# Optimization experiments

Measured on AMD Instinct MI355X. Metric: run time of the kernel, lower is better.

The kernel has to match this reference:

```python
import jax, jax.numpy as jnp
import numpy as np

DIM_CAP = 16   # capsule dim
NCLS = 17      # annotation_nr
BS = 16
T = 120        # chunk_size * fps
P = 22         # players per frame graph
G = BS * T     # number of graphs = 1920
N = G * P      # nodes = 42240
C_IN = 14
CHS = [16, 32, 64, 152]  # 8m,16m,32m,76m with m=2
BN_EPS = 1e-3


def _build_graph():
    # fully-connected directed edges within each 22-node graph (no self loops)
    ii, jj = np.meshgrid(np.arange(P), np.arange(P), indexing='ij')
    mask = ii != jj
    li, lj = ii[mask], jj[mask]               # (462,)
    base = (np.arange(G) * P)[:, None]
    src = (base + li[None, :]).reshape(-1)
    dst = (base + lj[None, :]).reshape(-1)
    edge_index = np.stack([src, dst]).astype(np.int64)   # (2, E)
    batch = np.repeat(np.arange(G), P).astype(np.int64)  # (N,)
    return jnp.asarray(edge_index), jnp.asarray(batch)


def setup_inputs() -> dict:
    key = jax.random.key(0)
    ks = jax.random.split(key, 16)
    edge_index, batch = _build_graph()
    E = edge_index.shape[1]
    x = jax.random.normal(ks[0], (N, C_IN), dtype=jnp.float32)
    edge_attr = jax.random.uniform(ks[1], (E, 5), dtype=jnp.float32)
    dims = [C_IN] + CHS
    params = {}
    for i in range(4):
        s = 1.0 / np.sqrt(dims[i])
        params[f'W{i+1}'] = jax.random.normal(ks[2 + i], (dims[i], dims[i + 1]), dtype=jnp.float32) * s
        params[f'b{i+1}'] = jnp.zeros((dims[i + 1],), dtype=jnp.float32)
    c_out = DIM_CAP * NCLS  # 272
    params['conv_w'] = jax.random.normal(ks[6], (c_out, CHS[-1], 3), dtype=jnp.float32) * (1.0 / np.sqrt(CHS[-1] * 3))
    params['conv_b'] = jnp.zeros((c_out,), dtype=jnp.float32)
    params['bn_gamma'] = jnp.ones((T,), dtype=jnp.float32)
    params['bn_beta'] = jnp.zeros((T,), dtype=jnp.float32)
    return dict(x=x, edge_index=edge_index, batch=batch, edge_attr=edge_attr, **params)


def _gcn_layer(x, src, dst, w_edge, W, b):
    # PyG GCNConv: x' = D^-1/2 (A + I) D^-1/2 (x W) + b, edge weights w, self-loop weight 1
    n = x.shape[0]
    h = x @ W
    loop = jnp.arange(n)
    src_f = jnp.concatenate([src, loop])
    dst_f = jnp.concatenate([dst, loop])
    w_f = jnp.concatenate([w_edge, jnp.ones((n,), h.dtype)])
    deg = jax.ops.segment_sum(w_f, dst_f, num_segments=n)
    dinv = jnp.where(deg > 0, jax.lax.rsqrt(deg), 0.0)
    norm = dinv[src_f] * w_f * dinv[dst_f]
    out = jax.ops.segment_sum(norm[:, None] * h[src_f], dst_f, num_segments=n)
    return out + b


def reference(x, edge_index, batch, edge_attr, W1, b1, W2, b2, W3, b3, W4, b4,
              conv_w, conv_b, bn_gamma, bn_beta):
    src, dst = edge_index[0], edge_index[1]
    ew = edge_attr[:, 4]
    h = jax.nn.relu(_gcn_layer(x, src, dst, ew, W1, b1))
    h = jax.nn.relu(_gcn_layer(h, src, dst, ew, W2, b2))
    h = jax.nn.relu(_gcn_layer(h, src, dst, ew, W3, b3))
    h = jax.nn.relu(_gcn_layer(h, src, dst, ew, W4, b4))
    # global mean pool per graph -> (G, 152)
    ones = jnp.ones((h.shape[0],), h.dtype)
    cnt = jax.ops.segment_sum(ones, batch, num_segments=G)
    pooled = jax.ops.segment_sum(h, batch, num_segments=G) / jnp.clip(cnt, 1.0)[:, None]
    # (BS, T, 152) -> (BS, 152, T); conv kernel (3,1) with pad (1,1) on T
    feat = pooled.reshape(BS, T, CHS[-1]).transpose(0, 2, 1)
    conv = jax.lax.conv_general_dilated(
        feat, conv_w, window_strides=(1,), padding=[(1, 1)],
        dimension_numbers=('NCH', 'OIH', 'NCH'))
    conv = conv + conv_b[None, :, None]            # (BS, 272, T)
    caps = conv.transpose(0, 2, 1).reshape(BS, T, DIM_CAP, NCLS)
    # BatchNorm2d(num_features=T) in eval mode: running mean 0, var 1
    scale = (bn_gamma / jnp.sqrt(1.0 + BN_EPS))[None, :, None, None]
    shift = bn_beta[None, :, None, None]
    s = jax.nn.sigmoid(caps * scale + shift)
    out = jnp.sqrt(jnp.sum(jnp.square(s - 0.5), axis=2) * 4.0 / DIM_CAP)
    return out  # (BS, T, NCLS)
```

## Files before the change

### kernel.cpp

```cpp
#include <hip/hip_runtime.h>
#include <hip/hip_bf16.h>

#define P22 22
#define PP 24
#define GROUPS 1920
#define CH4 152

template<int DIN, int DOUT, int PR1, int CR1, int PR2, int CR2>
__device__ __forceinline__ void gcn_layer(const float* __restrict__ W,
                                          const float* __restrict__ B,
                                          float* buf, float* T,
                                          const float* M, int tid)
{
    constexpr int NCT1 = DOUT / CR1;
    constexpr int NPT1 = PP / PR1;
    static_assert(NCT1 * NPT1 <= 256, "phase1 tiles must fit one round");
    if (tid < NCT1 * NPT1) {
        const int pt = tid / NCT1, ct = tid - pt * NCT1;
        const int p0 = pt * PR1, c0 = ct * CR1;
        float acc[PR1][CR1];
        #pragma unroll
        for (int a = 0; a < PR1; ++a)
            #pragma unroll
            for (int b = 0; b < CR1; ++b) acc[a][b] = 0.f;
        #pragma unroll 2
        for (int k = 0; k < DIN; ++k) {
            float xv[PR1], wv[CR1];
            #pragma unroll
            for (int a = 0; a < PR1; ++a) xv[a] = buf[k * PP + p0 + a];
            #pragma unroll
            for (int b = 0; b < CR1; ++b) wv[b] = W[k * DOUT + c0 + b];
            #pragma unroll
            for (int a = 0; a < PR1; ++a)
                #pragma unroll
                for (int b = 0; b < CR1; ++b)
                    acc[a][b] = fmaf(xv[a], wv[b], acc[a][b]);
        }
        #pragma unroll
        for (int a = 0; a < PR1; ++a)
            #pragma unroll
            for (int b = 0; b < CR1; ++b)
                T[(p0 + a) * DOUT + c0 + b] = acc[a][b];
    }
    __syncthreads();

    constexpr int NPT2 = PP / PR2;
    constexpr int NCT2 = DOUT / CR2;
    static_assert(NPT2 * NCT2 <= 256, "phase2 tiles must fit one round");
    if (tid < NPT2 * NCT2) {
        const int ct = tid / NPT2, pt = tid - ct * NPT2;
        const int p0 = pt * PR2, c0 = ct * CR2;
        float acc[CR2][PR2];
        #pragma unroll
        for (int b = 0; b < CR2; ++b) {
            const float bias = B[c0 + b];
            #pragma unroll
            for (int a = 0; a < PR2; ++a) acc[b][a] = bias;
        }
        #pragma unroll 2
        for (int q = 0; q < P22; ++q) {
            float av[PR2], tv[CR2];
            #pragma unroll
            for (int a = 0; a < PR2; ++a) av[a] = M[q * PP + p0 + a];
            #pragma unroll
            for (int b = 0; b < CR2; ++b) tv[b] = T[q * DOUT + c0 + b];
            #pragma unroll
            for (int b = 0; b < CR2; ++b)
                #pragma unroll
                for (int a = 0; a < PR2; ++a)
                    acc[b][a] = fmaf(av[a], tv[b], acc[b][a]);
        }
        #pragma unroll
        for (int b = 0; b < CR2; ++b)
            #pragma unroll
            for (int a = 0; a < PR2; ++a)
                buf[(c0 + b) * PP + p0 + a] = fmaxf(acc[b][a], 0.f);
    }
    __syncthreads();
}

__global__ __launch_bounds__(256) void gcn_kernel(
    const float* __restrict__ x, const float* __restrict__ ea,
    const float* __restrict__ W1, const float* __restrict__ b1,
    const float* __restrict__ W2, const float* __restrict__ b2,
    const float* __restrict__ W3, const float* __restrict__ b3,
    const float* __restrict__ W4, const float* __restrict__ b4,
    float* __restrict__ pooled)
{
    __shared__ __align__(16) float M[PP * PP];
    __shared__ __align__(16) float dinv[PP];
    __shared__ __align__(16) float buf[CH4 * PP];
    __shared__ __align__(16) float T[PP * CH4];

    const int g = blockIdx.x, tid = threadIdx.x;

    for (int idx = tid; idx < PP * PP; idx += 256) {
        int i = idx / PP, j = idx - i * PP;
        float v = 0.f;
        if (i < P22 && j < P22) {
            if (i == j) v = 1.0f;
            else {
                int e = i * 21 + j - (j > i);
                v = ea[((size_t)g * 462 + e) * 5 + 4];
            }
        }
        M[idx] = v;
    }
    for (int idx = tid; idx < 14 * PP; idx += 256) {
        int k = idx / PP, p = idx - k * PP;
        buf[idx] = (p < P22) ? x[((size_t)g * P22 + p) * 14 + k] : 0.f;
    }
    __syncthreads();

    if (tid < PP) {
        float s = 0.f;
        #pragma unroll
        for (int i = 0; i < P22; ++i) s += M[i * PP + tid];
        dinv[tid] = (s > 0.f) ? rsqrtf(s) : 0.f;
    }
    __syncthreads();
    for (int e = tid; e < PP * PP; e += 256) {
        int i = e / PP, j = e - i * PP;
        M[e] *= dinv[i] * dinv[j];
    }
    __syncthreads();

    gcn_layer<14, 16,  1, 2, 2, 1>(W1, b1, buf, T, M, tid);
    gcn_layer<16, 32,  1, 4, 2, 2>(W2, b2, buf, T, M, tid);
    gcn_layer<32, 64,  2, 4, 4, 2>(W3, b3, buf, T, M, tid);
    gcn_layer<64, 152, 4, 4, 4, 4>(W4, b4, buf, T, M, tid);

    for (int c = tid; c < CH4; c += 256) {
        float s = 0.f;
        #pragma unroll
        for (int p = 0; p < P22; ++p) s += buf[c * PP + p];
        pooled[(size_t)g * CH4 + c] = s * (1.0f / 22.0f);
    }
}

__global__ __launch_bounds__(256) void repack_conv_w(const float* __restrict__ cw,
                                                     float* __restrict__ wT)
{
    int idx = blockIdx.x * 256 + threadIdx.x;
    if (idx < 272 * 456) {
        int o = idx / 456, r = idx - o * 456;
        wT[r * 272 + o] = cw[idx];
    }
}

__global__ __launch_bounds__(320) void conv_caps_kernel(
    const float* __restrict__ pooled, const float* __restrict__ wT,
    const float* __restrict__ cb, const float* __restrict__ gamma,
    const float* __restrict__ beta, float* __restrict__ out)
{
    __shared__ __align__(16) float ftile[CH4 * 12];
    __shared__ __align__(16) float s2[8 * 272];
    __shared__ float sc[8], sh[8];

    const int bx = blockIdx.x;
    const int b = bx / 15, tile = bx - b * 15;
    const int t0 = tile * 8;
    const int tid = threadIdx.x;

    for (int idx = tid; idx < CH4 * 12; idx += 320) {
        int r = idx / CH4, i = idx - r * CH4;
        int t = t0 - 1 + r;
        float v = 0.f;
        if (r < 10 && t >= 0 && t < 120) v = pooled[((size_t)b * 120 + t) * CH4 + i];
        ftile[i * 12 + r] = v;
    }
    if (tid < 8) {
        int t = t0 + tid;
        sc[tid] = gamma[t] * 0.999500374688f;
        sh[tid] = beta[t];
    }
    __syncthreads();

    if (tid < 272) {
        const int o = tid;
        const float cb0 = cb[o];
        float acc[8];
        #pragma unroll
        for (int tt = 0; tt < 8; ++tt) acc[tt] = cb0;
        const float* wp0 = wT + o;
        float w0 = wp0[0], w1 = wp0[272], w2 = wp0[544];
        #pragma unroll 2
        for (int i = 0; i < CH4; ++i) {
            const int inext = (i == CH4 - 1) ? i : i + 1;
            const float* nwp = wp0 + inext * 816;
            float nw0 = nwp[0], nw1 = nwp[272], nw2 = nwp[544];
            const float4* fp = (const float4*)(ftile + i * 12);
            float4 f0 = fp[0], f1 = fp[1], f2 = fp[2];
            float fr[10] = { f0.x, f0.y, f0.z, f0.w, f1.x, f1.y, f1.z, f1.w, f2.x, f2.y };
            #pragma unroll
            for (int tt = 0; tt < 8; ++tt)
                acc[tt] = fmaf(w0, fr[tt], fmaf(w1, fr[tt + 1], fmaf(w2, fr[tt + 2], acc[tt])));
            w0 = nw0; w1 = nw1; w2 = nw2;
        }
        #pragma unroll
        for (int tt = 0; tt < 8; ++tt) {
            float z = fmaf(acc[tt], sc[tt], sh[tt]);
            float s = 1.0f / (1.0f + __expf(-z));
            float d = s - 0.5f;
            s2[tt * 272 + o] = d * d;
        }
    }
    __syncthreads();

    for (int e = tid; e < 8 * 17; e += 320) {
        int tt = e / 17, n = e - tt * 17;
        float s = 0.f;
        #pragma unroll
        for (int d = 0; d < 16; ++d) s += s2[tt * 272 + d * 17 + n];
        out[((size_t)b * 120 + t0 + tt) * 17 + n] = sqrtf(s) * 0.5f;
    }
}

extern "C" void kernel_launch(void* const* d_in, const int* in_sizes, int n_in,
                              void* d_out, int out_size, void* d_ws, size_t ws_size,
                              hipStream_t stream) {
    const float* x     = (const float*)d_in[0];
    const float* ea    = (const float*)d_in[3];
    const float* W1    = (const float*)d_in[4];
    const float* b1    = (const float*)d_in[5];
    const float* W2    = (const float*)d_in[6];
    const float* b2    = (const float*)d_in[7];
    const float* W3    = (const float*)d_in[8];
    const float* b3    = (const float*)d_in[9];
    const float* W4    = (const float*)d_in[10];
    const float* b4    = (const float*)d_in[11];
    const float* cw    = (const float*)d_in[12];
    const float* cb    = (const float*)d_in[13];
    const float* gamma = (const float*)d_in[14];
    const float* beta  = (const float*)d_in[15];
    float* out = (float*)d_out;

    float* pooled = (float*)d_ws;
    float* wT     = pooled + GROUPS * CH4;

    hipLaunchKernelGGL(repack_conv_w, dim3((272 * 456 + 255) / 256), dim3(256), 0, stream,
                       cw, wT);
    hipLaunchKernelGGL(gcn_kernel, dim3(GROUPS), dim3(256), 0, stream,
                       x, ea, W1, b1, W2, b2, W3, b3, W4, b4, pooled);
    hipLaunchKernelGGL(conv_caps_kernel, dim3(16 * 15), dim3(320), 0, stream,
                       pooled, wT, cb, gamma, beta, out);
}
```

Baseline: 172.3 us.

## Batch four graphs per block, reorder aggregation before weight matmul, fuse pooling

Each block now processes four graphs and applies the normalized adjacency before the weight multiply ((A X) W instead of A (X W)). It uses 8-wide float4 register tiles and fuses ReLU plus mean pooling into the last layer's epilogue. Pooled features are written transposed and padded so the conv kernel reads them straight from global memory without a shared staging tile. The goal is fewer blocks, fewer barriers, better reuse of the weights and adjacency per block, and no conv staging, at the cost of a larger shared-memory footprint and more register pressure.

Result: no change. 169.3 us (-1.7%).

```diff
diff --git a/kernel.cpp b/kernel.cpp
--- a/kernel.cpp
+++ b/kernel.cpp
@@ -1,82 +1,104 @@
 #include <hip/hip_runtime.h>
 #include <hip/hip_bf16.h>
 
-#define P22 22
-#define PP 24
 #define GROUPS 1920
 #define CH4 152
-
-template<int DIN, int DOUT, int PR1, int CR1, int PR2, int CR2>
-__device__ __forceinline__ void gcn_layer(const float* __restrict__ W,
-                                          const float* __restrict__ B,
-                                          float* buf, float* T,
-                                          const float* M, int tid)
-{
-    constexpr int NCT1 = DOUT / CR1;
-    constexpr int NPT1 = PP / PR1;
-    static_assert(NCT1 * NPT1 <= 256, "phase1 tiles must fit one round");
-    if (tid < NCT1 * NPT1) {
-        const int pt = tid / NCT1, ct = tid - pt * NCT1;
-        const int p0 = pt * PR1, c0 = ct * CR1;
-        float acc[PR1][CR1];
-        #pragma unroll
-        for (int a = 0; a < PR1; ++a)
-            #pragma unroll
-            for (int b = 0; b < CR1; ++b) acc[a][b] = 0.f;
+#define BUFS 100
+
+template<int DIN, int KR>
+__device__ __forceinline__ void layerA(const float* buf, float* Ut,
+                                       const float* A4, int tid)
+{
+    constexpr int NKT = DIN / KR;
+    constexpr int NT = NKT * 12;
+    if (tid < NT) {
+        const int kt = tid / 12, pt = tid - kt * 12;
+        const int g = pt / 3, ps = (pt - g * 3) * 8;
+        const int col0 = g * 24 + ps;
+        const int xcol = g * 24;
+        float acc[KR][8];
+        #pragma unroll
+        for (int j = 0; j < KR; ++j)
+            #pragma unroll
+            for (int a = 0; a < 8; ++a) acc[j][a] = 0.f;
         #pragma unroll 2
+        for (int q = 0; q < 22; ++q) {
+            const float4 a0 = *(const float4*)(A4 + (q * 4 + g) * 28 + ps);
+            const float4 a1 = *(const float4*)(A4 + (q * 4 + g) * 28 + ps + 4);
+            float xv[KR];
+            #pragma unroll
+            for (int j = 0; j < KR; ++j) xv[j] = buf[(kt * KR + j) * BUFS + xcol + q];
+            #pragma unroll
+            for (int j = 0; j < KR; ++j) {
+                acc[j][0] = fmaf(xv[j], a0.x, acc[j][0]);
+                acc[j][1] = fmaf(xv[j], a0.y, acc[j][1]);
+                acc[j][2] = fmaf(xv[j], a0.z, acc[j][2]);
+                acc[j][3] = fmaf(xv[j], a0.w, acc[j][3]);
+                acc[j][4] = fmaf(xv[j], a1.x, acc[j][4]);
+                acc[j][5] = fmaf(xv[j], a1.y, acc[j][5]);
+                acc[j][6] = fmaf(xv[j], a1.z, acc[j][6]);
+                acc[j][7] = fmaf(xv[j], a1.w, acc[j][7]);
+            }
+        }
+        #pragma unroll
+        for (int j = 0; j < KR; ++j) {
+            *(float4*)(Ut + (kt * KR + j) * BUFS + col0) =
+                make_float4(acc[j][0], acc[j][1], acc[j][2], acc[j][3]);
+            *(float4*)(Ut + (kt * KR + j) * BUFS + col0 + 4) =
+                make_float4(acc[j][4], acc[j][5], acc[j][6], acc[j][7]);
+        }
+    }
+}
+
+template<int DIN, int DOUT, int CR>
+__device__ __forceinline__ void layerB(const float* __restrict__ W,
+                                       const float* __restrict__ B,
+                                       const float* Ut, float* buf, int tid)
+{
+    constexpr int NCT = DOUT / CR;
+    constexpr int NT = NCT * 12;
+    if (tid < NT) {
+        const int ct = tid / 12, pt = tid - ct * 12;
+        const int p0 = pt * 8, c0 = ct * CR;
+        float acc[CR][8];
+        #pragma unroll
+        for (int b = 0; b < CR; ++b) {
+            const float bias = B[c0 + b];
+            #pragma unroll
+            for (int a = 0; a < 8; ++a) acc[b][a] = bias;
+        }
+        #pragma unroll 4
         for (int k = 0; k < DIN; ++k) {
-            float xv[PR1], wv[CR1];
-            #pragma unroll
-            for (int a = 0; a < PR1; ++a) xv[a] = buf[k * PP + p0 + a];
-            #pragma unroll
-            for (int b = 0; b < CR1; ++b) wv[b] = W[k * DOUT + c0 + b];
-            #pragma unroll
-            for (int a = 0; a < PR1; ++a)
-                #pragma unroll
-                for (int b = 0; b < CR1; ++b)
-                    acc[a][b] = fmaf(xv[a], wv[b], acc[a][b]);
-        }
-        #pragma unroll
-        for (int a = 0; a < PR1; ++a)
-            #pragma unroll
-            for (int b = 0; b < CR1; ++b)
-                T[(p0 + a) * DOUT + c0 + b] = acc[a][b];
-    }
-    __syncthreads();
-
-    constexpr int NPT2 = PP / PR2;
-    constexpr int NCT2 = DOUT / CR2;
-    static_assert(NPT2 * NCT2 <= 256, "phase2 tiles must fit one round");
-    if (tid < NPT2 * NCT2) {
-        const int ct = tid / NPT2, pt = tid - ct * NPT2;
-        const int p0 = pt * PR2, c0 = ct * CR2;
-        float acc[CR2][PR2];
-        #pragma unroll
-        for (int b = 0; b < CR2; ++b) {
-            const float bias = B[c0 + b];
-            #pragma unroll
-            for (int a = 0; a < PR2; ++a) acc[b][a] = bias;
-        }
-        #pragma unroll 2
-        for (int q = 0; q < P22; ++q) {
-            float av[PR2], tv[CR2];
-            #pragma unroll
-            for (int a = 0; a < PR2; ++a) av[a] = M[q * PP + p0 + a];
-            #pragma unroll
-            for (int b = 0; b < CR2; ++b) tv[b] = T[q * DOUT + c0 + b];
-            #pragma unroll
-            for (int b = 0; b < CR2; ++b)
-                #pragma unroll
-                for (int a = 0; a < PR2; ++a)
-                    acc[b][a] = fmaf(av[a], tv[b], acc[b][a]);
-        }
-        #pragma unroll
-        for (int b = 0; b < CR2; ++b)
-            #pragma unroll
-            for (int a = 0; a < PR2; ++a)
-                buf[(c0 + b) * PP + p0 + a] = fmaxf(acc[b][a], 0.f);
-    }
-    __syncthreads();
+            const float4 u0 = *(const float4*)(Ut + k * BUFS + p0);
+            const float4 u1 = *(const float4*)(Ut + k * BUFS + p0 + 4);
+            float wv[CR];
+            #pragma unroll
+            for (int b = 0; b < CR; b += 4) {
+                const float4 w4 = *(const float4*)(W + k * DOUT + c0 + b);
+                wv[b] = w4.x; wv[b + 1] = w4.y; wv[b + 2] = w4.z; wv[b + 3] = w4.w;
+            }
+            #pragma unroll
+            for (int b = 0; b < CR; ++b) {
+                acc[b][0] = fmaf(wv[b], u0.x, acc[b][0]);
+                acc[b][1] = fmaf(wv[b], u0.y, acc[b][1]);
+                acc[b][2] = fmaf(wv[b], u0.z, acc[b][2]);
+                acc[b][3] = fmaf(wv[b], u0.w, acc[b][3]);
+                acc[b][4] = fmaf(wv[b], u1.x, acc[b][4]);
+                acc[b][5] = fmaf(wv[b], u1.y, acc[b][5]);
+                acc[b][6] = fmaf(wv[b], u1.z, acc[b][6]);
+                acc[b][7] = fmaf(wv[b], u1.w, acc[b][7]);
+            }
+        }
+        #pragma unroll
+        for (int b = 0; b < CR; ++b) {
+            *(float4*)(buf + (c0 + b) * BUFS + p0) =
+                make_float4(fmaxf(acc[b][0], 0.f), fmaxf(acc[b][1], 0.f),
+                            fmaxf(acc[b][2], 0.f), fmaxf(acc[b][3], 0.f));
+            *(float4*)(buf + (c0 + b) * BUFS + p0 + 4) =
+                make_float4(fmaxf(acc[b][4], 0.f), fmaxf(acc[b][5], 0.f),
+                            fmaxf(acc[b][6], 0.f), fmaxf(acc[b][7], 0.f));
+        }
+    }
 }
 
 __global__ __launch_bounds__(256) void gcn_kernel(
@@ -85,75 +107,144 @@
     const float* __restrict__ W2, const float* __restrict__ b2,
     const float* __restrict__ W3, const float* __restrict__ b3,
     const float* __restrict__ W4, const float* __restrict__ b4,
-    float* __restrict__ pooled)
-{
-    __shared__ __align__(16) float M[PP * PP];
-    __shared__ __align__(16) float dinv[PP];
-    __shared__ __align__(16) float buf[CH4 * PP];
-    __shared__ __align__(16) float T[PP * CH4];
-
-    const int g = blockIdx.x, tid = threadIdx.x;
-
-    for (int idx = tid; idx < PP * PP; idx += 256) {
-        int i = idx / PP, j = idx - i * PP;
+    float* __restrict__ pooledT)
+{
+    __shared__ __align__(16) float A4[24 * 4 * 28];
+    __shared__ __align__(16) float dv[4 * 24];
+    __shared__ __align__(16) float buf[64 * BUFS];
+    __shared__ __align__(16) float Ut[64 * BUFS];
+
+    const int tid = threadIdx.x;
+    const int G0 = blockIdx.x * 4;
+
+    for (int idx = tid; idx < 24 * 4 * 28; idx += 256) {
+        const int q = idx / 112, r = idx - q * 112;
+        const int g = r / 28, p = r - g * 28;
         float v = 0.f;
-        if (i < P22 && j < P22) {
-            if (i == j) v = 1.0f;
+        if (q < 22 && p < 22) {
+            if (q == p) v = 1.0f;
             else {
-                int e = i * 21 + j - (j > i);
-                v = ea[((size_t)g * 462 + e) * 5 + 4];
-            }
-        }
-        M[idx] = v;
-    }
-    for (int idx = tid; idx < 14 * PP; idx += 256) {
-        int k = idx / PP, p = idx - k * PP;
-        buf[idx] = (p < P22) ? x[((size_t)g * P22 + p) * 14 + k] : 0.f;
-    }
-    __syncthreads();
-
-    if (tid < PP) {
+                const int e = q * 21 + p - (p > q);
+                v = ea[((size_t)(G0 + g) * 462 + e) * 5 + 4];
+            }
+        }
+        A4[idx] = v;
+    }
+    for (int idx = tid; idx < 14 * 96; idx += 256) {
+        const int k = idx / 96, col = idx - k * 96;
+        const int g = col / 24, p = col - g * 24;
+        buf[k * BUFS + col] = (p < 22) ? x[((size_t)(G0 + g) * 22 + p) * 14 + k] : 0.f;
+    }
+    __syncthreads();
+
+    if (tid < 96) {
+        const int g = tid / 24, p = tid - g * 24;
         float s = 0.f;
         #pragma unroll
-        for (int i = 0; i < P22; ++i) s += M[i * PP + tid];
-        dinv[tid] = (s > 0.f) ? rsqrtf(s) : 0.f;
-    }
-    __syncthreads();
-    for (int e = tid; e < PP * PP; e += 256) {
-        int i = e / PP, j = e - i * PP;
-        M[e] *= dinv[i] * dinv[j];
-    }
-    __syncthreads();
-
-    gcn_layer<14, 16,  1, 2, 2, 1>(W1, b1, buf, T, M, tid);
-    gcn_layer<16, 32,  1, 4, 2, 2>(W2, b2, buf, T, M, tid);
-    gcn_layer<32, 64,  2, 4, 4, 2>(W3, b3, buf, T, M, tid);
-    gcn_layer<64, 152, 4, 4, 4, 4>(W4, b4, buf, T, M, tid);
-
-    for (int c = tid; c < CH4; c += 256) {
-        float s = 0.f;
-        #pragma unroll
-        for (int p = 0; p < P22; ++p) s += buf[c * PP + p];
-        pooled[(size_t)g * CH4 + c] = s * (1.0f / 22.0f);
+        for (int q = 0; q < 22; ++q) s += A4[(q * 4 + g) * 28 + p];
+        dv[tid] = (s > 0.f) ? rsqrtf(s) : 0.f;
+    }
+    __syncthreads();
+    for (int idx = tid; idx < 24 * 4 * 28; idx += 256) {
+        const int q = idx / 112, r = idx - q * 112;
+        const int g = r / 28, p = r - g * 28;
+        if (p < 24) A4[idx] *= dv[g * 24 + q] * dv[g * 24 + p];
+    }
+    __syncthreads();
+
+    layerA<14, 2>(buf, Ut, A4, tid);  __syncthreads();
+    layerB<14, 16, 4>(W1, b1, Ut, buf, tid);  __syncthreads();
+    layerA<16, 4>(buf, Ut, A4, tid);  __syncthreads();
+    layerB<16, 32, 4>(W2, b2, Ut, buf, tid);  __syncthreads();
+    layerA<32, 4>(buf, Ut, A4, tid);  __syncthreads();
+    layerB<32, 64, 8>(W3, b3, Ut, buf, tid);  __syncthreads();
+    layerA<64, 4>(buf, Ut, A4, tid);  __syncthreads();
+
+    float* pscr = buf;
+    if (tid < 19 * 12) {
+        const int ct = tid / 12, pt = tid - ct * 12;
+        const int p0 = pt * 8, c0 = ct * 8;
+        float acc[8][8];
+        #pragma unroll
+        for (int b = 0; b < 8; ++b) {
+            const float bias = b4[c0 + b];
+            #pragma unroll
+            for (int a = 0; a < 8; ++a) acc[b][a] = bias;
+        }
+        #pragma unroll 4
+        for (int k = 0; k < 64; ++k) {
+            const float4 u0 = *(const float4*)(Ut + k * BUFS + p0);
+            const float4 u1 = *(const float4*)(Ut + k * BUFS + p0 + 4);
+            float wv[8];
+            #pragma unroll
+            for (int b = 0; b < 8; b += 4) {
+                const float4 w4 = *(const float4*)(W4 + k * 152 + c0 + b);
+                wv[b] = w4.x; wv[b + 1] = w4.y; wv[b + 2] = w4.z; wv[b + 3] = w4.w;
+            }
+            #pragma unroll
+            for (int b = 0; b < 8; ++b) {
+                acc[b][0] = fmaf(wv[b], u0.x, acc[b][0]);
+                acc[b][1] = fmaf(wv[b], u0.y, acc[b][1]);
+                acc[b][2] = fmaf(wv[b], u0.z, acc[b][2]);
+                acc[b][3] = fmaf(wv[b], u0.w, acc[b][3]);
+                acc[b][4] = fmaf(wv[b], u1.x, acc[b][4]);
+                acc[b][5] = fmaf(wv[b], u1.y, acc[b][5]);
+                acc[b][6] = fmaf(wv[b], u1.z, acc[b][6]);
+                acc[b][7] = fmaf(wv[b], u1.w, acc[b][7]);
+            }
+        }
+        const int alim = ((pt % 3) == 2) ? 6 : 8;
+        float ps8[8];
+        #pragma unroll
+        for (int b = 0; b < 8; ++b) {
+            float s = 0.f;
+            #pragma unroll
+            for (int a = 0; a < 8; ++a)
+                s += (a < alim) ? fmaxf(acc[b][a], 0.f) : 0.f;
+            ps8[b] = s;
+        }
+        *(float4*)(pscr + pt * 152 + c0) = make_float4(ps8[0], ps8[1], ps8[2], ps8[3]);
+        *(float4*)(pscr + pt * 152 + c0 + 4) = make_float4(ps8[4], ps8[5], ps8[6], ps8[7]);
+    }
+    __syncthreads();
+
+    if (tid < 152) {
+        const int c = tid;
+        const int b = G0 / 120, t0 = G0 - b * 120;
+        float4 v;
+        #pragma unroll
+        for (int g = 0; g < 4; ++g) {
+            const float s = pscr[(g * 3 + 0) * 152 + c] + pscr[(g * 3 + 1) * 152 + c]
+                          + pscr[(g * 3 + 2) * 152 + c];
+            ((float*)&v)[g] = s * (1.0f / 22.0f);
+        }
+        *(float4*)(pooledT + ((size_t)(b * 152 + c) * 128) + 4 + t0) = v;
     }
 }
 
 __global__ __launch_bounds__(256) void repack_conv_w(const float* __restrict__ cw,
-                                                     float* __restrict__ wT)
-{
-    int idx = blockIdx.x * 256 + threadIdx.x;
+                                                     float* __restrict__ wT,
+                                                     float* __restrict__ pT)
+{
+    const int idx = blockIdx.x * 256 + threadIdx.x;
     if (idx < 272 * 456) {
-        int o = idx / 456, r = idx - o * 456;
+        const int o = idx / 456, r = idx - o * 456;
         wT[r * 272 + o] = cw[idx];
+    } else {
+        const int j = idx - 272 * 456;
+        if (j < 16 * 152 * 8) {
+            const int row = j >> 3, s = j & 7;
+            const int slot = (s < 4) ? s : s + 120;
+            pT[(size_t)row * 128 + slot] = 0.f;
+        }
     }
 }
 
 __global__ __launch_bounds__(320) void conv_caps_kernel(
-    const float* __restrict__ pooled, const float* __restrict__ wT,
+    const float* __restrict__ pT, const float* __restrict__ wT,
     const float* __restrict__ cb, const float* __restrict__ gamma,
     const float* __restrict__ beta, float* __restrict__ out)
 {
-    __shared__ __align__(16) float ftile[CH4 * 12];
     __shared__ __align__(16) float s2[8 * 272];
     __shared__ float sc[8], sh[8];
 
@@ -162,15 +253,8 @@
     const int t0 = tile * 8;
     const int tid = threadIdx.x;
 
-    for (int idx = tid; idx < CH4 * 12; idx += 320) {
-        int r = idx / CH4, i = idx - r * CH4;
-        int t = t0 - 1 + r;
-        float v = 0.f;
-        if (r < 10 && t >= 0 && t < 120) v = pooled[((size_t)b * 120 + t) * CH4 + i];
-        ftile[i * 12 + r] = v;
-    }
     if (tid < 8) {
-        int t = t0 + tid;
+        const int t = t0 + tid;
         sc[tid] = gamma[t] * 0.999500374688f;
         sh[tid] = beta[t];
     }
@@ -183,15 +267,17 @@
         #pragma unroll
         for (int tt = 0; tt < 8; ++tt) acc[tt] = cb0;
         const float* wp0 = wT + o;
+        const float* frow0 = pT + ((size_t)b * 152) * 128 + 3 + t0;
         float w0 = wp0[0], w1 = wp0[272], w2 = wp0[544];
         #pragma unroll 2
         for (int i = 0; i < CH4; ++i) {
             const int inext = (i == CH4 - 1) ? i : i + 1;
             const float* nwp = wp0 + inext * 816;
-            float nw0 = nwp[0], nw1 = nwp[272], nw2 = nwp[544];
-            const float4* fp = (const float4*)(ftile + i * 12);
-            float4 f0 = fp[0], f1 = fp[1], f2 = fp[2];
-            float fr[10] = { f0.x, f0.y, f0.z, f0.w, f1.x, f1.y, f1.z, f1.w, f2.x, f2.y };
+            const float nw0 = nwp[0], nw1 = nwp[272], nw2 = nwp[544];
+            const float* f = frow0 + (size_t)i * 128;
+            float fr[10];
+            #pragma unroll
+            for (int j = 0; j < 10; ++j) fr[j] = f[j];
             #pragma unroll
             for (int tt = 0; tt < 8; ++tt)
                 acc[tt] = fmaf(w0, fr[tt], fmaf(w1, fr[tt + 1], fmaf(w2, fr[tt + 2], acc[tt])));
@@ -199,16 +285,16 @@
         }
         #pragma unroll
         for (int tt = 0; tt < 8; ++tt) {
-            float z = fmaf(acc[tt], sc[tt], sh[tt]);
-            float s = 1.0f / (1.0f + __expf(-z));
-            float d = s - 0.5f;
+            const float z = fmaf(acc[tt], sc[tt], sh[tt]);
+            const float s = 1.0f / (1.0f + __expf(-z));
+            const float d = s - 0.5f;
             s2[tt * 272 + o] = d * d;
         }
     }
     __syncthreads();
 
     for (int e = tid; e < 8 * 17; e += 320) {
-        int tt = e / 17, n = e - tt * 17;
+        const int tt = e / 17, n = e - tt * 17;
         float s = 0.f;
         #pragma unroll
         for (int d = 0; d < 16; ++d) s += s2[tt * 272 + d * 17 + n];
@@ -235,13 +321,13 @@
     const float* beta  = (const float*)d_in[15];
     float* out = (float*)d_out;
 
-    float* pooled = (float*)d_ws;
-    float* wT     = pooled + GROUPS * CH4;
-
-    hipLaunchKernelGGL(repack_conv_w, dim3((272 * 456 + 255) / 256), dim3(256), 0, stream,
-                       cw, wT);
-    hipLaunchKernelGGL(gcn_kernel, dim3(GROUPS), dim3(256), 0, stream,
-                       x, ea, W1, b1, W2, b2, W3, b3, W4, b4, pooled);
+    float* pT = (float*)d_ws;
+    float* wT = pT + (size_t)16 * 152 * 128;
+
+    hipLaunchKernelGGL(repack_conv_w, dim3((272 * 456 + 16 * 152 * 8 + 255) / 256),
+                       dim3(256), 0, stream, cw, wT, pT);
+    hipLaunchKernelGGL(gcn_kernel, dim3(GROUPS / 4), dim3(256), 0, stream,
+                       x, ea, W1, b1, W2, b2, W3, b3, W4, b4, pT);
     hipLaunchKernelGGL(conv_caps_kernel, dim3(16 * 15), dim3(320), 0, stream,
-                       pooled, wT, cb, gamma, beta, out);
-}
+                       pT, wT, cb, gamma, beta, out);
+}
```
